# Kernel optimization log

Hardware: AMD Instinct MI355X
Metric: run time of the kernel (lower is better)

The kernel has to match this reference:

```python
import jax, jax.numpy as jnp
import numpy as np

NG = 100000   # number of g-side nodes
NS = 100000   # number of s-side nodes
E = 640000    # edges per direction
D = 128       # feature / embed dim


def setup_inputs() -> dict:
    key = jax.random.key(0)
    ks = jax.random.split(key, 16)
    inp = {
        'Xg_self':  jax.random.normal(ks[0], (NG, D), jnp.float32),
        'Xs_self':  jax.random.normal(ks[1], (NS, D), jnp.float32),
        'Xs_for_g': jax.random.normal(ks[2], (NS, D), jnp.float32),
        'Xg_for_s': jax.random.normal(ks[3], (NG, D), jnp.float32),
        # COO edge lists for the two bipartite sparse adjacencies
        'row_gs': jax.random.randint(ks[4], (E,), 0, NG, jnp.int32),
        'col_gs': jax.random.randint(ks[5], (E,), 0, NS, jnp.int32),
        'val_gs': jax.random.uniform(ks[6], (E,), jnp.float32),
        'row_sg': jax.random.randint(ks[7], (E,), 0, NS, jnp.int32),
        'col_sg': jax.random.randint(ks[8], (E,), 0, NG, jnp.int32),
        'val_sg': jax.random.uniform(ks[9], (E,), jnp.float32),
        # Linear weights (PyTorch layout: [out_features, in_features], no bias)
        'Wg_self':  jax.random.normal(ks[10], (D, D), jnp.float32) * 0.05,
        'Wg_neigh': jax.random.normal(ks[11], (D, D), jnp.float32) * 0.05,
        'Ws_self':  jax.random.normal(ks[12], (D, D), jnp.float32) * 0.05,
        'Ws_neigh': jax.random.normal(ks[13], (D, D), jnp.float32) * 0.05,
    }
    return inp


def reference(Xg_self, Xs_self, Xs_for_g, Xg_for_s,
              row_gs, col_gs, val_gs, row_sg, col_sg, val_sg,
              Wg_self, Wg_neigh, Ws_self, Ws_neigh):
    # SpMM: neigh_g = A_gs @ Xs_for_g  (Ng x Ns sparse times Ns x D dense)
    neigh_g = jax.ops.segment_sum(Xs_for_g[col_gs] * val_gs[:, None], row_gs,
                                  num_segments=NG)
    # SpMM: neigh_s = A_sg @ Xg_for_s
    neigh_s = jax.ops.segment_sum(Xg_for_s[col_sg] * val_sg[:, None], row_sg,
                                  num_segments=NS)
    out_g = jax.nn.relu(Xg_self @ Wg_self.T + neigh_g @ Wg_neigh.T)
    out_s = jax.nn.relu(Xs_self @ Ws_self.T + neigh_s @ Ws_neigh.T)
    return (out_g, out_s)
```

## Files before the change

kernel.cpp:

```cpp
#include <hip/hip_runtime.h>
#include <hip/hip_bf16.h>
#include <stdint.h>

typedef __attribute__((ext_vector_type(4))) float f32x4;
typedef __attribute__((ext_vector_type(2))) float f32x2;
typedef __attribute__((ext_vector_type(8))) short bf16x8;

#define D 128

__device__ inline short f2bf(float x) {
    __hip_bfloat16 h = __float2bfloat16(x);
    return __builtin_bit_cast(short, h);
}

__device__ inline bf16x8 pack8(f32x4 lo, f32x4 hi) {
    bf16x8 b;
    b[0] = f2bf(lo[0]); b[1] = f2bf(lo[1]); b[2] = f2bf(lo[2]); b[3] = f2bf(lo[3]);
    b[4] = f2bf(hi[0]); b[5] = f2bf(hi[1]); b[6] = f2bf(hi[2]); b[7] = f2bf(hi[3]);
    return b;
}

__device__ inline unsigned int pack2bf(float a, float b) {
    unsigned int ua = (unsigned int)(unsigned short)f2bf(a);
    unsigned int ub = (unsigned int)(unsigned short)f2bf(b);
    return ua | (ub << 16);
}


__global__ __launch_bounds__(256)
void xprep_kernel(const float* __restrict__ src, unsigned short* __restrict__ dst, int n8)
{
    int i = blockIdx.x * 256 + threadIdx.x;
    if (i >= n8) return;
    f32x4 lo = *reinterpret_cast<const f32x4*>(src + (size_t)i * 8);
    f32x4 hi = *reinterpret_cast<const f32x4*>(src + (size_t)i * 8 + 4);
    *reinterpret_cast<bf16x8*>(dst + (size_t)i * 8) = pack8(lo, hi);
}


__global__ __launch_bounds__(256)
void wprep_kernel(const float* __restrict__ Wg_self, const float* __restrict__ Wg_neigh,
                  const float* __restrict__ Ws_self, const float* __restrict__ Ws_neigh,
                  short* __restrict__ Wcat)
{
    int t = blockIdx.x * 256 + threadIdx.x;
    if (t >= 2 * 128 * 32) return;
    int dir = t >> 12;
    int rem = t & 4095;
    int j = rem >> 5;
    int k = (rem & 31) * 8;
    const float* Wself  = dir ? Ws_self  : Wg_self;
    const float* Wneigh = dir ? Ws_neigh : Wg_neigh;
    const float* src = (k < 128) ? (Wself + j * D + k) : (Wneigh + j * D + (k - 128));
    f32x4 lo = *reinterpret_cast<const f32x4*>(src);
    f32x4 hi = *reinterpret_cast<const f32x4*>(src + 4);
    *reinterpret_cast<bf16x8*>(Wcat + (size_t)dir * 32768 + j * 256 + k) = pack8(lo, hi);
}


__global__ __launch_bounds__(256)
void hist2_kernel(const int* __restrict__ rowA, int EA,
                  const int* __restrict__ rowB, int NGoff,
                  int* __restrict__ cnt, int Etot)
{
    int e = blockIdx.x * 256 + threadIdx.x;
    if (e >= Etot) return;
    int r = (e < EA) ? rowA[e] : (rowB[e - EA] + NGoff);
    atomicAdd(&cnt[r], 1);
}

__global__ __launch_bounds__(256)
void scan1_kernel(const int* __restrict__ cnt, int* __restrict__ part,
                  int* __restrict__ blksums, int N)
{
    __shared__ int wsum[4];
    int t = threadIdx.x;
    int base = blockIdx.x * 1024 + t * 4;
    int v0 = base + 0 < N ? cnt[base + 0] : 0;
    int v1 = base + 1 < N ? cnt[base + 1] : 0;
    int v2 = base + 2 < N ? cnt[base + 2] : 0;
    int v3 = base + 3 < N ? cnt[base + 3] : 0;
    int s = v0 + v1 + v2 + v3;
    int lane = t & 63, w = t >> 6;
    int x = s;
#pragma unroll
    for (int off = 1; off < 64; off <<= 1) {
        int y = __shfl_up(x, off);
        if (lane >= off) x += y;
    }
    if (lane == 63) wsum[w] = x;
    __syncthreads();
    int woff = 0;
    for (int i = 0; i < w; ++i) woff += wsum[i];
    int incl = x + woff;
    int excl = incl - s;
    if (base + 0 < N) part[base + 0] = excl;
    if (base + 1 < N) part[base + 1] = excl + v0;
    if (base + 2 < N) part[base + 2] = excl + v0 + v1;
    if (base + 3 < N) part[base + 3] = excl + v0 + v1 + v2;
    if (t == 255) blksums[blockIdx.x] = incl;
}

__global__ __launch_bounds__(256)
void scan2_kernel(int* __restrict__ blksums, int nb)
{
    __shared__ int wsum[4];
    int t = threadIdx.x;
    int v = t < nb ? blksums[t] : 0;
    int lane = t & 63, w = t >> 6;
    int x = v;
#pragma unroll
    for (int off = 1; off < 64; off <<= 1) {
        int y = __shfl_up(x, off);
        if (lane >= off) x += y;
    }
    if (lane == 63) wsum[w] = x;
    __syncthreads();
    int woff = 0;
    for (int i = 0; i < w; ++i) woff += wsum[i];
    int excl = x + woff - v;
    if (t < nb) blksums[t] = excl;
}

__global__ __launch_bounds__(256)
void scan3_kernel(int* __restrict__ start, int* __restrict__ cursor,
                  const int* __restrict__ blksums, int N)
{
    int i = blockIdx.x * 256 + threadIdx.x;
    if (i < N) {
        int v = start[i] + blksums[i >> 10];
        start[i] = v;
        cursor[i] = v;
    }
}

__global__ __launch_bounds__(256)
void fill2_kernel(const int* __restrict__ rowA, const int* __restrict__ colA,
                  const float* __restrict__ valA, int EA,
                  const int* __restrict__ rowB, const int* __restrict__ colB,
                  const float* __restrict__ valB, int NGoff,
                  int* __restrict__ cursor, int2* __restrict__ pairs, int Etot)
{
    int e = blockIdx.x * 256 + threadIdx.x;
    if (e >= Etot) return;
    int r, c; float v;
    if (e < EA) { r = rowA[e]; c = colA[e]; v = valA[e]; }
    else { int e2 = e - EA; r = rowB[e2] + NGoff; c = colB[e2]; v = valB[e2]; }
    int p = atomicAdd(&cursor[r], 1);
    pairs[p] = make_int2(c, __float_as_int(v));
}

__global__ __launch_bounds__(256)
void fused_kernel(const unsigned short* __restrict__ X16_0,
                  const unsigned short* __restrict__ X16_1,
                  const float* __restrict__ Xself0, float* __restrict__ out0, int n0,
                  const float* __restrict__ Xself1, float* __restrict__ out1, int n1,
                  const int* __restrict__ start, const int* __restrict__ cnt,
                  const int2* __restrict__ pairs, const short* __restrict__ Wcat)
{
    __shared__ bf16x8 Ab[32 * 32];
    const int ROWS = 32;
    int blocks0 = (n0 + ROWS - 1) / ROWS;

    const unsigned short* X16; const float* Xself; float* out;
    int nRows, r0base, csr0; const short* Wb;
    if ((int)blockIdx.x < blocks0) {
        X16 = X16_0; Xself = Xself0; out = out0; nRows = n0;
        r0base = blockIdx.x * ROWS; csr0 = 0; Wb = Wcat;
    } else {
        X16 = X16_1; Xself = Xself1; out = out1; nRows = n1;
        r0base = ((int)blockIdx.x - blocks0) * ROWS; csr0 = n0; Wb = Wcat + 32768;
    }

    const int tid = threadIdx.x, wave = tid >> 6, lane = tid & 63;
    const int l15 = lane & 15, lhi = lane >> 4;
    const int l31 = lane & 31, half = lane >> 5;

    unsigned int* Aw   = (unsigned int*)Ab;
    uint2*        A64  = (uint2*)Ab;

#pragma unroll 1
    for (int i = 0; i < 4; ++i) {
        int r = wave * 8 + i * 2 + half;
        int R = r0base + r;
        if (R >= nRows) R = nRows - 1;
        int gid = csr0 + R;
        int s = start[gid];
        int n = cnt[gid];
        f32x4 acc = {0.f, 0.f, 0.f, 0.f};
        int j = 0;
        for (; j + 4 <= n; j += 4) {
            int2 p[4]; uint2 xb[4];
#pragma unroll
            for (int u = 0; u < 4; ++u) {
                p[u] = pairs[s + j + u];
                xb[u] = *reinterpret_cast<const uint2*>(X16 + (size_t)p[u].x * D + l31 * 4);
            }
#pragma unroll
            for (int u = 0; u < 4; ++u) {
                float v = __int_as_float(p[u].y);
                acc[0] += __uint_as_float(xb[u].x << 16) * v;
                acc[1] += __uint_as_float(xb[u].x & 0xffff0000u) * v;
                acc[2] += __uint_as_float(xb[u].y << 16) * v;
                acc[3] += __uint_as_float(xb[u].y & 0xffff0000u) * v;
            }
        }
        for (; j < n; ++j) {
            int2 p = pairs[s + j];
            uint2 xb = *reinterpret_cast<const uint2*>(X16 + (size_t)p.x * D + l31 * 4);
            float v = __int_as_float(p.y);
            acc[0] += __uint_as_float(xb.x << 16) * v;
            acc[1] += __uint_as_float(xb.x & 0xffff0000u) * v;
            acc[2] += __uint_as_float(xb.y << 16) * v;
            acc[3] += __uint_as_float(xb.y & 0xffff0000u) * v;
        }
        f32x4 xs = *reinterpret_cast<const f32x4*>(Xself + (size_t)R * D + l31 * 4);
        uint2 sb = { pack2bf(xs[0], xs[1]),  pack2bf(xs[2], xs[3]) };
        uint2 nb = { pack2bf(acc[0], acc[1]), pack2bf(acc[2], acc[3]) };
        int rx = r & 7;
        int cS = (l31 >> 1) ^ rx;
        int cN = 16 + ((l31 >> 1) ^ rx);
        A64[r * 64 + cS * 2 + (l31 & 1)] = sb;
        A64[r * 64 + cN * 2 + (l31 & 1)] = nb;
    }

    bf16x8 bfrag[2][8];
#pragma unroll
    for (int n = 0; n < 2; ++n) {
        int j = wave * 32 + n * 16 + l15;
#pragma unroll
        for (int kb = 0; kb < 8; ++kb)
            bfrag[n][kb] = *reinterpret_cast<const bf16x8*>(
                Wb + (size_t)j * 256 + kb * 32 + lhi * 8);
    }

    __syncthreads();

#pragma unroll
    for (int it = 0; it < 2; ++it) {
        int r = it * 16 + l15;
        int rx = r & 7;
        f32x4 acc0 = {0.f, 0.f, 0.f, 0.f};
        f32x4 acc1 = {0.f, 0.f, 0.f, 0.f};
#pragma unroll
        for (int kb = 0; kb < 8; ++kb) {
            int c = kb * 4 + lhi;
            bf16x8 af = Ab[r * 32 + (c ^ rx)];
            acc0 = __builtin_amdgcn_mfma_f32_16x16x32_bf16(af, bfrag[0][kb], acc0, 0, 0, 0);
            acc1 = __builtin_amdgcn_mfma_f32_16x16x32_bf16(af, bfrag[1][kb], acc1, 0, 0, 0);
        }
#pragma unroll
        for (int i2 = 0; i2 < 4; ++i2) {
            int rr = r0base + it * 16 + lhi * 4 + i2;
            if (rr < nRows) {
                float v0 = acc0[i2] > 0.f ? acc0[i2] : 0.f;
                float v1 = acc1[i2] > 0.f ? acc1[i2] : 0.f;
                out[(size_t)rr * D + wave * 32 + l15]      = v0;
                out[(size_t)rr * D + wave * 32 + 16 + l15] = v1;
            }
        }
    }
}


__global__ __launch_bounds__(256)
void scatter_edges(const float* __restrict__ X, const int* __restrict__ row,
                   const int* __restrict__ col, const float* __restrict__ val,
                   float* out, int nE)
{
    int t = blockIdx.x * 256 + threadIdx.x;
    int e = t >> 5;
    if (e >= nE) return;
    int l = t & 31;
    int r = row[e];
    int c = col[e];
    float v = val[e];
    f32x4 x = *reinterpret_cast<const f32x4*>(X + (size_t)c * D + l * 4);
    float* o = out + (size_t)r * D + l * 4;
    unsafeAtomicAdd(o + 0, x[0] * v);
    unsafeAtomicAdd(o + 1, x[1] * v);
    unsafeAtomicAdd(o + 2, x[2] * v);
    unsafeAtomicAdd(o + 3, x[3] * v);
}

__global__ __launch_bounds__(256)
void gemm_relu_fb(const float* __restrict__ Xself, const float* __restrict__ Neigh,
                  const float* __restrict__ Wself, const float* __restrict__ Wneigh,
                  float* __restrict__ out, int nRows)
{
    const int tid  = threadIdx.x;
    const int wave = tid >> 6;
    const int lane = tid & 63;
    const int l15  = lane & 15;
    const int lhi  = lane >> 4;

    bf16x8 bfrag[2][8];
#pragma unroll
    for (int n = 0; n < 2; ++n) {
        int j = wave * 32 + n * 16 + l15;
#pragma unroll
        for (int kb = 0; kb < 8; ++kb) {
            int k = kb * 32 + lhi * 8;
            const float* src = (kb < 4) ? (Wself + j * D + k)
                                        : (Wneigh + j * D + (k - 128));
            f32x4 lo = *reinterpret_cast<const f32x4*>(src);
            f32x4 hi = *reinterpret_cast<const f32x4*>(src + 4);
            bfrag[n][kb] = pack8(lo, hi);
        }
    }

    int r0base = blockIdx.x * 128;
#pragma unroll 1
    for (int it = 0; it < 8; ++it) {
        int r0 = r0base + it * 16;
        if (r0 >= nRows) break;
        const float* xrow = Xself + (size_t)(r0 + l15) * D;
        const float* nrow = Neigh + (size_t)(r0 + l15) * D;
        bf16x8 afrag[8];
#pragma unroll
        for (int kb = 0; kb < 8; ++kb) {
            const float* src = (kb < 4) ? (xrow + kb * 32 + lhi * 8)
                                        : (nrow + (kb - 4) * 32 + lhi * 8);
            f32x4 lo = *reinterpret_cast<const f32x4*>(src);
            f32x4 hi = *reinterpret_cast<const f32x4*>(src + 4);
            afrag[kb] = pack8(lo, hi);
        }
        asm volatile("s_waitcnt vmcnt(0)" ::: "memory");
        __syncthreads();

        f32x4 acc0 = {0.f, 0.f, 0.f, 0.f};
        f32x4 acc1 = {0.f, 0.f, 0.f, 0.f};
#pragma unroll
        for (int kb = 0; kb < 8; ++kb) {
            acc0 = __builtin_amdgcn_mfma_f32_16x16x32_bf16(afrag[kb], bfrag[0][kb], acc0, 0, 0, 0);
            acc1 = __builtin_amdgcn_mfma_f32_16x16x32_bf16(afrag[kb], bfrag[1][kb], acc1, 0, 0, 0);
        }
#pragma unroll
        for (int i = 0; i < 4; ++i) {
            int rr = r0 + lhi * 4 + i;
            if (rr < nRows) {
                float v0 = acc0[i] > 0.f ? acc0[i] : 0.f;
                float v1 = acc1[i] > 0.f ? acc1[i] : 0.f;
                out[(size_t)rr * D + wave * 32 + l15]      = v0;
                out[(size_t)rr * D + wave * 32 + 16 + l15] = v1;
            }
        }
    }
}


extern "C" void kernel_launch(void* const* d_in, const int* in_sizes, int n_in,
                              void* d_out, int out_size, void* d_ws, size_t ws_size,
                              hipStream_t stream)
{
    const float* Xg_self  = (const float*)d_in[0];
    const float* Xs_self  = (const float*)d_in[1];
    const float* Xs_for_g = (const float*)d_in[2];
    const float* Xg_for_s = (const float*)d_in[3];
    const int*   row_gs   = (const int*)d_in[4];
    const int*   col_gs   = (const int*)d_in[5];
    const float* val_gs   = (const float*)d_in[6];
    const int*   row_sg   = (const int*)d_in[7];
    const int*   col_sg   = (const int*)d_in[8];
    const float* val_sg   = (const float*)d_in[9];
    const float* Wg_self  = (const float*)d_in[10];
    const float* Wg_neigh = (const float*)d_in[11];
    const float* Ws_self  = (const float*)d_in[12];
    const float* Ws_neigh = (const float*)d_in[13];

    const int NG = in_sizes[0] / D;
    const int NS = in_sizes[1] / D;
    const int E1 = in_sizes[4];
    const int E2 = in_sizes[7];
    const int N  = NG + NS;
    const int Etot = E1 + E2;

    float* out_g = (float*)d_out;
    float* out_s = out_g + (size_t)NG * D;

    size_t off = 0;
    auto alloc = [&](size_t bytes) -> size_t {
        off = (off + 255) & ~(size_t)255;
        size_t o = off;
        off += bytes;
        return o;
    };
    size_t x16g_o   = alloc(sizeof(short) * (size_t)NG * D);
    size_t x16s_o   = alloc(sizeof(short) * (size_t)NS * D);
    size_t wcat_o   = alloc(sizeof(short) * 2 * 128 * 256);
    size_t cnt_o    = alloc(sizeof(int) * N);
    size_t start_o  = alloc(sizeof(int) * N);
    size_t cursor_o = alloc(sizeof(int) * N);
    size_t pairs_o  = alloc(sizeof(int2) * (size_t)Etot);
    size_t blk_o    = alloc(sizeof(int) * 1024);
    size_t need_bytes = off;

    char* ws = (char*)d_ws;

    if (ws_size < need_bytes) {
        hipMemsetAsync(d_out, 0, (size_t)out_size * sizeof(float), stream);
        {
            long long threads = (long long)E1 * 32;
            scatter_edges<<<(int)((threads + 255) / 256), 256, 0, stream>>>(
                Xs_for_g, row_gs, col_gs, val_gs, out_g, E1);
        }
        {
            long long threads = (long long)E2 * 32;
            scatter_edges<<<(int)((threads + 255) / 256), 256, 0, stream>>>(
                Xg_for_s, row_sg, col_sg, val_sg, out_s, E2);
        }
        gemm_relu_fb<<<(NG + 127) / 128, 256, 0, stream>>>(Xg_self, out_g, Wg_self, Wg_neigh, out_g, NG);
        gemm_relu_fb<<<(NS + 127) / 128, 256, 0, stream>>>(Xs_self, out_s, Ws_self, Ws_neigh, out_s, NS);
        return;
    }

    unsigned short* x16g = (unsigned short*)(ws + x16g_o);
    unsigned short* x16s = (unsigned short*)(ws + x16s_o);
    short* wcat  = (short*)(ws + wcat_o);
    int* cnt     = (int*)(ws + cnt_o);
    int* start   = (int*)(ws + start_o);
    int* cursor  = (int*)(ws + cursor_o);
    int2* pairs  = (int2*)(ws + pairs_o);
    int* blk     = (int*)(ws + blk_o);

    xprep_kernel<<<(NG * D / 8 + 255) / 256, 256, 0, stream>>>(Xs_for_g, x16g, NG * D / 8);
    xprep_kernel<<<(NS * D / 8 + 255) / 256, 256, 0, stream>>>(Xg_for_s, x16s, NS * D / 8);
    wprep_kernel<<<32, 256, 0, stream>>>(Wg_self, Wg_neigh, Ws_self, Ws_neigh, wcat);

    hipMemsetAsync(cnt, 0, sizeof(int) * N, stream);
    hist2_kernel<<<(Etot + 255) / 256, 256, 0, stream>>>(row_gs, E1, row_sg, NG, cnt, Etot);
    int nb = (N + 1023) / 1024;
    scan1_kernel<<<nb, 256, 0, stream>>>(cnt, start, blk, N);
    scan2_kernel<<<1, 256, 0, stream>>>(blk, nb);
    scan3_kernel<<<(N + 255) / 256, 256, 0, stream>>>(start, cursor, blk, N);
    fill2_kernel<<<(Etot + 255) / 256, 256, 0, stream>>>(
        row_gs, col_gs, val_gs, E1, row_sg, col_sg, val_sg, NG, cursor, pairs, Etot);

    int blocks0 = (NG + 31) / 32, blocks1 = (NS + 31) / 32;
    fused_kernel<<<blocks0 + blocks1, 256, 0, stream>>>(
        x16g, x16s,
        Xg_self, out_g, NG,
        Xs_self, out_s, NS,
        start, cnt, pairs, wcat);
}
```

Measured before the change: 319.0 us.

## Merge prep kernels, drop start array, widen fused kernel to 512 threads

Merges the X and W bf16 conversion and the row histogram into one prep kernel, which cuts launches. The separate start array goes away: after fill the cursor holds row ends, so start is recovered as end minus count. The fused kernel moves to 512 threads with one 16-column tile per wave and eight-way unrolled gather with clamped tails. It also stages Xself into LDS with global_load_lds, swizzled to avoid bank conflicts, and packs it to bf16 at MFMA operand time. The risks are higher register pressure under the (512,6) launch bounds and extra work in padded tail iterations.

```diff
diff --git a/kernel.cpp b/kernel.cpp
--- a/kernel.cpp
+++ b/kernel.cpp
@@ -3,10 +3,11 @@
 #include <stdint.h>
 
 typedef __attribute__((ext_vector_type(4))) float f32x4;
-typedef __attribute__((ext_vector_type(2))) float f32x2;
 typedef __attribute__((ext_vector_type(8))) short bf16x8;
 
 #define D 128
+#define GLOBAL_AS __attribute__((address_space(1)))
+#define LDS_AS __attribute__((address_space(3)))
 
 __device__ inline short f2bf(float x) {
     __hip_bfloat16 h = __float2bfloat16(x);
@@ -28,46 +29,51 @@
 
 
 __global__ __launch_bounds__(256)
-void xprep_kernel(const float* __restrict__ src, unsigned short* __restrict__ dst, int n8)
-{
-    int i = blockIdx.x * 256 + threadIdx.x;
-    if (i >= n8) return;
-    f32x4 lo = *reinterpret_cast<const f32x4*>(src + (size_t)i * 8);
-    f32x4 hi = *reinterpret_cast<const f32x4*>(src + (size_t)i * 8 + 4);
-    *reinterpret_cast<bf16x8*>(dst + (size_t)i * 8) = pack8(lo, hi);
-}
-
-
-__global__ __launch_bounds__(256)
-void wprep_kernel(const float* __restrict__ Wg_self, const float* __restrict__ Wg_neigh,
-                  const float* __restrict__ Ws_self, const float* __restrict__ Ws_neigh,
-                  short* __restrict__ Wcat)
+void prep_kernel(const float* __restrict__ Xa, const float* __restrict__ Xb,
+                 unsigned short* __restrict__ x16a, unsigned short* __restrict__ x16b,
+                 const float* __restrict__ Wg_self, const float* __restrict__ Wg_neigh,
+                 const float* __restrict__ Ws_self, const float* __restrict__ Ws_neigh,
+                 short* __restrict__ Wcat,
+                 const int* __restrict__ rowA, int EA,
+                 const int* __restrict__ rowB, int NGoff,
+                 int* __restrict__ cnt,
+                 int n8a, int n8b, int Etot)
 {
     int t = blockIdx.x * 256 + threadIdx.x;
-    if (t >= 2 * 128 * 32) return;
-    int dir = t >> 12;
-    int rem = t & 4095;
-    int j = rem >> 5;
-    int k = (rem & 31) * 8;
-    const float* Wself  = dir ? Ws_self  : Wg_self;
-    const float* Wneigh = dir ? Ws_neigh : Wg_neigh;
-    const float* src = (k < 128) ? (Wself + j * D + k) : (Wneigh + j * D + (k - 128));
-    f32x4 lo = *reinterpret_cast<const f32x4*>(src);
-    f32x4 hi = *reinterpret_cast<const f32x4*>(src + 4);
-    *reinterpret_cast<bf16x8*>(Wcat + (size_t)dir * 32768 + j * 256 + k) = pack8(lo, hi);
-}
-
-
-__global__ __launch_bounds__(256)
-void hist2_kernel(const int* __restrict__ rowA, int EA,
-                  const int* __restrict__ rowB, int NGoff,
-                  int* __restrict__ cnt, int Etot)
-{
-    int e = blockIdx.x * 256 + threadIdx.x;
-    if (e >= Etot) return;
-    int r = (e < EA) ? rowA[e] : (rowB[e - EA] + NGoff);
-    atomicAdd(&cnt[r], 1);
-}
+    if (t < n8a) {
+        f32x4 lo = *reinterpret_cast<const f32x4*>(Xa + (size_t)t * 8);
+        f32x4 hi = *reinterpret_cast<const f32x4*>(Xa + (size_t)t * 8 + 4);
+        *reinterpret_cast<bf16x8*>(x16a + (size_t)t * 8) = pack8(lo, hi);
+        return;
+    }
+    t -= n8a;
+    if (t < n8b) {
+        f32x4 lo = *reinterpret_cast<const f32x4*>(Xb + (size_t)t * 8);
+        f32x4 hi = *reinterpret_cast<const f32x4*>(Xb + (size_t)t * 8 + 4);
+        *reinterpret_cast<bf16x8*>(x16b + (size_t)t * 8) = pack8(lo, hi);
+        return;
+    }
+    t -= n8b;
+    if (t < 2 * 128 * 32) {
+        int dir = t >> 12;
+        int rem = t & 4095;
+        int j = rem >> 5;
+        int k = (rem & 31) * 8;
+        const float* Wself  = dir ? Ws_self  : Wg_self;
+        const float* Wneigh = dir ? Ws_neigh : Wg_neigh;
+        const float* src = (k < 128) ? (Wself + j * D + k) : (Wneigh + j * D + (k - 128));
+        f32x4 lo = *reinterpret_cast<const f32x4*>(src);
+        f32x4 hi = *reinterpret_cast<const f32x4*>(src + 4);
+        *reinterpret_cast<bf16x8*>(Wcat + (size_t)dir * 32768 + j * 256 + k) = pack8(lo, hi);
+        return;
+    }
+    t -= 2 * 128 * 32;
+    if (t < Etot) {
+        int r = (t < EA) ? rowA[t] : (rowB[t - EA] + NGoff);
+        atomicAdd(&cnt[r], 1);
+    }
+}
+
 
 __global__ __launch_bounds__(256)
 void scan1_kernel(const int* __restrict__ cnt, int* __restrict__ part,
@@ -123,15 +129,10 @@
 }
 
 __global__ __launch_bounds__(256)
-void scan3_kernel(int* __restrict__ start, int* __restrict__ cursor,
-                  const int* __restrict__ blksums, int N)
+void scan3_kernel(int* __restrict__ cursor, const int* __restrict__ blksums, int N)
 {
     int i = blockIdx.x * 256 + threadIdx.x;
-    if (i < N) {
-        int v = start[i] + blksums[i >> 10];
-        start[i] = v;
-        cursor[i] = v;
-    }
+    if (i < N) cursor[i] += blksums[i >> 10];
 }
 
 __global__ __launch_bounds__(256)
@@ -150,15 +151,17 @@
     pairs[p] = make_int2(c, __float_as_int(v));
 }
 
-__global__ __launch_bounds__(256)
+__global__ __launch_bounds__(512, 6)
 void fused_kernel(const unsigned short* __restrict__ X16_0,
                   const unsigned short* __restrict__ X16_1,
                   const float* __restrict__ Xself0, float* __restrict__ out0, int n0,
                   const float* __restrict__ Xself1, float* __restrict__ out1, int n1,
-                  const int* __restrict__ start, const int* __restrict__ cnt,
+                  const int* __restrict__ cnt, const int* __restrict__ endpos,
                   const int2* __restrict__ pairs, const short* __restrict__ Wcat)
 {
-    __shared__ bf16x8 Ab[32 * 32];
+    __shared__ float  As[32 * 128];
+    __shared__ bf16x8 Ab[32 * 16];
+
     const int ROWS = 32;
     int blocks0 = (n0 + ROWS - 1) / ROWS;
 
@@ -172,65 +175,62 @@
         r0base = ((int)blockIdx.x - blocks0) * ROWS; csr0 = n0; Wb = Wcat + 32768;
     }
 
-    const int tid = threadIdx.x, wave = tid >> 6, lane = tid & 63;
-    const int l15 = lane & 15, lhi = lane >> 4;
-    const int l31 = lane & 31, half = lane >> 5;
-
-    unsigned int* Aw   = (unsigned int*)Ab;
-    uint2*        A64  = (uint2*)Ab;
-
+    const int tid  = threadIdx.x;
+    const int wave = tid >> 6, lane = tid & 63;
+    const int l15  = lane & 15, lhi = lane >> 4;
+    const int l31  = lane & 31;
+    const int hw   = tid >> 5;
+
+#pragma unroll
+    for (int q = 0; q < 2; ++q) {
+        int rs = wave * 4 + q * 2 + (lane >> 5);
+        int R = r0base + rs; if (R > nRows - 1) R = nRows - 1;
+        const float* g = Xself + (size_t)R * D + (((lane & 31) ^ (rs & 7)) << 2);
+        __builtin_amdgcn_global_load_lds((const GLOBAL_AS uint32_t*)g,
+                                         (LDS_AS uint32_t*)(&As[(wave * 4 + q * 2) * 128]),
+                                         16, 0, 0);
+    }
+
+    uint2* Ab64 = (uint2*)Ab;
 #pragma unroll 1
-    for (int i = 0; i < 4; ++i) {
-        int r = wave * 8 + i * 2 + half;
-        int R = r0base + r;
-        if (R >= nRows) R = nRows - 1;
+    for (int ii = 0; ii < 2; ++ii) {
+        int r = hw * 2 + ii;
+        int R = r0base + r; if (R > nRows - 1) R = nRows - 1;
         int gid = csr0 + R;
-        int s = start[gid];
         int n = cnt[gid];
+        int s = endpos[gid] - n;
         f32x4 acc = {0.f, 0.f, 0.f, 0.f};
-        int j = 0;
-        for (; j + 4 <= n; j += 4) {
-            int2 p[4]; uint2 xb[4];
-#pragma unroll
-            for (int u = 0; u < 4; ++u) {
-                p[u] = pairs[s + j + u];
+#pragma unroll 1
+        for (int j = 0; j < n; j += 8) {
+            int2 p[8]; uint2 xb[8];
+#pragma unroll
+            for (int u = 0; u < 8; ++u) {
+                int idx = (j + u < n) ? j + u : n - 1;
+                p[u] = pairs[s + idx];
+            }
+#pragma unroll
+            for (int u = 0; u < 8; ++u)
                 xb[u] = *reinterpret_cast<const uint2*>(X16 + (size_t)p[u].x * D + l31 * 4);
-            }
-#pragma unroll
-            for (int u = 0; u < 4; ++u) {
-                float v = __int_as_float(p[u].y);
+#pragma unroll
+            for (int u = 0; u < 8; ++u) {
+                float v = (j + u < n) ? __int_as_float(p[u].y) : 0.f;
                 acc[0] += __uint_as_float(xb[u].x << 16) * v;
                 acc[1] += __uint_as_float(xb[u].x & 0xffff0000u) * v;
                 acc[2] += __uint_as_float(xb[u].y << 16) * v;
                 acc[3] += __uint_as_float(xb[u].y & 0xffff0000u) * v;
             }
         }
-        for (; j < n; ++j) {
-            int2 p = pairs[s + j];
-            uint2 xb = *reinterpret_cast<const uint2*>(X16 + (size_t)p.x * D + l31 * 4);
-            float v = __int_as_float(p.y);
-            acc[0] += __uint_as_float(xb.x << 16) * v;
-            acc[1] += __uint_as_float(xb.x & 0xffff0000u) * v;
-            acc[2] += __uint_as_float(xb.y << 16) * v;
-            acc[3] += __uint_as_float(xb.y & 0xffff0000u) * v;
-        }
-        f32x4 xs = *reinterpret_cast<const f32x4*>(Xself + (size_t)R * D + l31 * 4);
-        uint2 sb = { pack2bf(xs[0], xs[1]),  pack2bf(xs[2], xs[3]) };
         uint2 nb = { pack2bf(acc[0], acc[1]), pack2bf(acc[2], acc[3]) };
-        int rx = r & 7;
-        int cS = (l31 >> 1) ^ rx;
-        int cN = 16 + ((l31 >> 1) ^ rx);
-        A64[r * 64 + cS * 2 + (l31 & 1)] = sb;
-        A64[r * 64 + cN * 2 + (l31 & 1)] = nb;
-    }
-
-    bf16x8 bfrag[2][8];
-#pragma unroll
-    for (int n = 0; n < 2; ++n) {
-        int j = wave * 32 + n * 16 + l15;
+        int cn = (l31 >> 1) ^ (r & 7);
+        Ab64[r * 32 + cn * 2 + (l31 & 1)] = nb;
+    }
+
+    bf16x8 bfrag[8];
+    {
+        int j = wave * 16 + l15;
 #pragma unroll
         for (int kb = 0; kb < 8; ++kb)
-            bfrag[n][kb] = *reinterpret_cast<const bf16x8*>(
+            bfrag[kb] = *reinterpret_cast<const bf16x8*>(
                 Wb + (size_t)j * 256 + kb * 32 + lhi * 8);
     }
 
@@ -240,23 +240,27 @@
     for (int it = 0; it < 2; ++it) {
         int r = it * 16 + l15;
         int rx = r & 7;
-        f32x4 acc0 = {0.f, 0.f, 0.f, 0.f};
-        f32x4 acc1 = {0.f, 0.f, 0.f, 0.f};
+        f32x4 acc = {0.f, 0.f, 0.f, 0.f};
 #pragma unroll
         for (int kb = 0; kb < 8; ++kb) {
-            int c = kb * 4 + lhi;
-            bf16x8 af = Ab[r * 32 + (c ^ rx)];
-            acc0 = __builtin_amdgcn_mfma_f32_16x16x32_bf16(af, bfrag[0][kb], acc0, 0, 0, 0);
-            acc1 = __builtin_amdgcn_mfma_f32_16x16x32_bf16(af, bfrag[1][kb], acc1, 0, 0, 0);
+            bf16x8 af;
+            if (kb < 4) {
+                int c0 = kb * 8 + lhi * 2;
+                f32x4 lo = *reinterpret_cast<const f32x4*>(&As[r * 128 + ((c0 ^ rx) << 2)]);
+                f32x4 hi = *reinterpret_cast<const f32x4*>(&As[r * 128 + (((c0 + 1) ^ rx) << 2)]);
+                af = pack8(lo, hi);
+            } else {
+                int cn = (kb - 4) * 4 + lhi;
+                af = Ab[r * 16 + (cn ^ rx)];
+            }
+            acc = __builtin_amdgcn_mfma_f32_16x16x32_bf16(af, bfrag[kb], acc, 0, 0, 0);
         }
 #pragma unroll
         for (int i2 = 0; i2 < 4; ++i2) {
             int rr = r0base + it * 16 + lhi * 4 + i2;
             if (rr < nRows) {
-                float v0 = acc0[i2] > 0.f ? acc0[i2] : 0.f;
-                float v1 = acc1[i2] > 0.f ? acc1[i2] : 0.f;
-                out[(size_t)rr * D + wave * 32 + l15]      = v0;
-                out[(size_t)rr * D + wave * 32 + 16 + l15] = v1;
+                float v = acc[i2] > 0.f ? acc[i2] : 0.f;
+                out[(size_t)rr * D + wave * 16 + l15] = v;
             }
         }
     }
@@ -389,7 +393,6 @@
     size_t x16s_o   = alloc(sizeof(short) * (size_t)NS * D);
     size_t wcat_o   = alloc(sizeof(short) * 2 * 128 * 256);
     size_t cnt_o    = alloc(sizeof(int) * N);
-    size_t start_o  = alloc(sizeof(int) * N);
     size_t cursor_o = alloc(sizeof(int) * N);
     size_t pairs_o  = alloc(sizeof(int2) * (size_t)Etot);
     size_t blk_o    = alloc(sizeof(int) * 1024);
@@ -418,28 +421,33 @@
     unsigned short* x16s = (unsigned short*)(ws + x16s_o);
     short* wcat  = (short*)(ws + wcat_o);
     int* cnt     = (int*)(ws + cnt_o);
-    int* start   = (int*)(ws + start_o);
     int* cursor  = (int*)(ws + cursor_o);
     int2* pairs  = (int2*)(ws + pairs_o);
     int* blk     = (int*)(ws + blk_o);
 
-    xprep_kernel<<<(NG * D / 8 + 255) / 256, 256, 0, stream>>>(Xs_for_g, x16g, NG * D / 8);
-    xprep_kernel<<<(NS * D / 8 + 255) / 256, 256, 0, stream>>>(Xg_for_s, x16s, NS * D / 8);
-    wprep_kernel<<<32, 256, 0, stream>>>(Wg_self, Wg_neigh, Ws_self, Ws_neigh, wcat);
+    const int n8a = NG * D / 8, n8b = NS * D / 8;
 
     hipMemsetAsync(cnt, 0, sizeof(int) * N, stream);
-    hist2_kernel<<<(Etot + 255) / 256, 256, 0, stream>>>(row_gs, E1, row_sg, NG, cnt, Etot);
+
+    {
+        long long tot = (long long)n8a + n8b + 2 * 128 * 32 + Etot;
+        prep_kernel<<<(int)((tot + 255) / 256), 256, 0, stream>>>(
+            Xs_for_g, Xg_for_s, x16g, x16s,
+            Wg_self, Wg_neigh, Ws_self, Ws_neigh, wcat,
+            row_gs, E1, row_sg, NG, cnt, n8a, n8b, Etot);
+    }
+
     int nb = (N + 1023) / 1024;
-    scan1_kernel<<<nb, 256, 0, stream>>>(cnt, start, blk, N);
+    scan1_kernel<<<nb, 256, 0, stream>>>(cnt, cursor, blk, N);
     scan2_kernel<<<1, 256, 0, stream>>>(blk, nb);
-    scan3_kernel<<<(N + 255) / 256, 256, 0, stream>>>(start, cursor, blk, N);
+    scan3_kernel<<<(N + 255) / 256, 256, 0, stream>>>(cursor, blk, N);
     fill2_kernel<<<(Etot + 255) / 256, 256, 0, stream>>>(
         row_gs, col_gs, val_gs, E1, row_sg, col_sg, val_sg, NG, cursor, pairs, Etot);
 
     int blocks0 = (NG + 31) / 32, blocks1 = (NS + 31) / 32;
-    fused_kernel<<<blocks0 + blocks1, 256, 0, stream>>>(
+    fused_kernel<<<blocks0 + blocks1, 512, 0, stream>>>(
         x16g, x16s,
         Xg_self, out_g, NG,
         Xs_self, out_s, NS,
-        start, cnt, pairs, wcat);
-}
+        cnt, cursor, pairs, wcat);
+}
```

Result: faster. 297.6 us (-6.7%).
